# Optimization experiments

Hardware: AMD Instinct MI355X
Metric: run time of the kernel (lower is better)

Reference implementation:

```python
import jax, jax.numpy as jnp
import numpy as np

NUM_LAYER = 3
LEAKY = 0.8
RES = 0.8  # residual scale in convolution


def spmm(row, col, val, x, n):
    # sparse (n x n) COO @ dense (n x d)
    return jax.ops.segment_sum(val[:, None] * x[col], row, num_segments=n)


def convolution(emb, row, col, val):
    n = emb.shape[0]
    all_e = emb
    acc = emb  # layer-0 term
    for _ in range(NUM_LAYER):
        all_e = spmm(row, col, val, all_e, n) + RES * all_e
        acc = acc + all_e
    return acc / (NUM_LAYER + 1)


def setup_inputs() -> dict:
    key = jax.random.key(0)
    ks = jax.random.split(key, 32)
    B, NU, NQ, NC, DE, DF = 16384, 50000, 20000, 512, 64, 128
    EU, EQ, EK = 1600000, 640000, 16384
    inp = {}
    inp['user_id'] = jax.random.randint(ks[0], (B,), 0, NU)
    inp['question_id'] = jax.random.randint(ks[1], (B,), 0, NQ)
    inp['q_table'] = (jax.random.uniform(ks[2], (NQ, NC)) < 0.05).astype(jnp.float32)
    inp['u_row'] = jax.random.randint(ks[3], (EU,), 0, NU)
    inp['u_col'] = jax.random.randint(ks[4], (EU,), 0, NU)
    inp['u_val'] = jax.random.uniform(ks[5], (EU,)) / 32.0
    inp['e_row'] = jax.random.randint(ks[6], (EQ,), 0, NQ)
    inp['e_col'] = jax.random.randint(ks[7], (EQ,), 0, NQ)
    inp['e_val'] = jax.random.uniform(ks[8], (EQ,)) / 32.0
    inp['k_row'] = jax.random.randint(ks[9], (EK,), 0, NC)
    inp['k_col'] = jax.random.randint(ks[10], (EK,), 0, NC)
    inp['k_val'] = jax.random.uniform(ks[11], (EK,)) / 32.0
    inp['student_emb'] = jax.random.normal(ks[12], (NU, DE)) * 0.1
    inp['exercise_emb'] = jax.random.normal(ks[13], (NQ, DE)) * 0.1
    inp['knowledge_emb'] = jax.random.normal(ks[14], (NC, DE)) * 0.1
    inp['W_s'] = jax.random.normal(ks[15], (DE, DF)) * 0.1
    inp['b_s'] = jnp.zeros((DF,))
    inp['W_e'] = jax.random.normal(ks[16], (DE, DF)) * 0.1
    inp['b_e'] = jnp.zeros((DF,))
    inp['W_k'] = jax.random.normal(ks[17], (DE, DF)) * 0.1
    inp['b_k'] = jnp.zeros((DF,))
    inp['W_d'] = jax.random.normal(ks[18], (DE, 1)) * 0.1
    inp['b_d'] = jnp.zeros((1,))
    inp['M1_w'] = jax.random.normal(ks[19], (NC, 512)) * 0.05
    inp['M1_b'] = jnp.zeros((512,))
    inp['M2_w'] = jax.random.normal(ks[20], (512, 256)) * 0.05
    inp['M2_b'] = jnp.zeros((256,))
    inp['M3_w'] = jax.random.normal(ks[21], (256, 128)) * 0.05
    inp['M3_b'] = jnp.zeros((128,))
    inp['M4_w'] = jax.random.normal(ks[22], (128, 1)) * 0.05
    inp['M4_b'] = jnp.zeros((1,))
    return inp


def reference(user_id, question_id, q_table,
              u_row, u_col, u_val, e_row, e_col, e_val, k_row, k_col, k_val,
              student_emb, exercise_emb, knowledge_emb,
              W_s, b_s, W_e, b_e, W_k, b_k, W_d, b_d,
              M1_w, M1_b, M2_w, M2_b, M3_w, M3_b, M4_w, M4_b):
    cs = convolution(student_emb, u_row, u_col, u_val)    # [NU, DE]
    ce = convolution(exercise_emb, e_row, e_col, e_val)   # [NQ, DE]
    ck = convolution(knowledge_emb, k_row, k_col, k_val)  # [NC, DE]
    bs = cs[user_id]        # [B, DE]
    be = ce[question_id]    # [B, DE]
    sf = jax.nn.leaky_relu(bs @ W_s + b_s, LEAKY)   # [B, DF]
    ef = jax.nn.leaky_relu(be @ W_e + b_e, LEAKY)   # [B, DF]
    kf = jax.nn.leaky_relu(ck @ W_k + b_k, LEAKY)   # [NC, DF]
    disc = jax.nn.sigmoid(be @ W_d + b_d)           # [B, 1]
    state = disc * ((sf - ef) @ kf.T) * q_table[question_id]  # [B, NC]
    h = jnp.tanh(state @ M1_w + M1_b)
    h = jnp.tanh(h @ M2_w + M2_b)
    h = jnp.tanh(h @ M3_w + M3_b)
    return jax.nn.sigmoid(h @ M4_w + M4_b).reshape(-1)  # [B]
```

## Files before the change

kernel.cpp:

```cpp
#include <hip/hip_runtime.h>
#include <hip/hip_bf16.h>
#include <math.h>

#define RESF 0.8f
#define LEAKYF 0.8f
#define BWSH 6
#define BWID 64
#define BSTRIDE 2432

typedef __attribute__((ext_vector_type(8))) short bs8;
typedef __attribute__((ext_vector_type(4))) float f32x4;

__device__ __forceinline__ void gload16(const void* g, void* l) {
  __builtin_amdgcn_global_load_lds((const __attribute__((address_space(1))) void*)g,
                                   (__attribute__((address_space(3))) void*)l, 16, 0, 0);
}

__device__ __forceinline__ float tanh_fast(float x) {
  float t = __expf(2.f * x);
  return 1.f - 2.f * __builtin_amdgcn_rcpf(1.f + t);
}
__device__ __forceinline__ float sigmoid_fast(float x) {
  return __builtin_amdgcn_rcpf(1.f + __expf(-x));
}
__device__ __forceinline__ float bf2f(ushort u) {
  return __uint_as_float((unsigned)u << 16);
}
__device__ __forceinline__ ushort f2bf(float a) {
  __hip_bfloat16 h = __float2bfloat16(a);
  return *(ushort*)&h;
}

__device__ __forceinline__ int edge_row(int e, const int* __restrict__ rU, const int* __restrict__ rE,
                                        const int* __restrict__ rK, int EU, int EQ, int NU, int NQ) {
  if (e < EU) return rU[e];
  if ((e -= EU) < EQ) return NU + rE[e];
  e -= EQ;
  return NU + NQ + rK[e];
}

__device__ __forceinline__ void edge_full(int e,
    const int* __restrict__ rU, const int* __restrict__ cU, const float* __restrict__ vU,
    const int* __restrict__ rE, const int* __restrict__ cE, const float* __restrict__ vE,
    const int* __restrict__ rK, const int* __restrict__ cK, const float* __restrict__ vK,
    int EU, int EQ, int NU, int NQ, int& grow, int& gcol, float& val) {
  if (e < EU) { grow = rU[e]; gcol = cU[e]; val = vU[e]; return; }
  if ((e -= EU) < EQ) { grow = NU + rE[e]; gcol = NU + cE[e]; val = vE[e]; return; }
  e -= EQ;
  grow = NU + NQ + rK[e]; gcol = NU + NQ + cK[e]; val = vK[e];
}

__global__ __launch_bounds__(256) void k_setup(int* __restrict__ gcur, int* __restrict__ flags,
                                               int* __restrict__ nneed, int nbuck, int N_tot) {
  int i = blockIdx.x * 256 + threadIdx.x;
  if (i < nbuck) gcur[i] = i * BSTRIDE;
  if (i < N_tot) flags[i] = 0;
  if (i == 0) nneed[0] = 0;
}

__global__ __launch_bounds__(1024) void k_bin(
    const int* __restrict__ rU, const int* __restrict__ cU, const float* __restrict__ vU,
    const int* __restrict__ rE, const int* __restrict__ cE, const float* __restrict__ vE,
    const int* __restrict__ rK, const int* __restrict__ cK, const float* __restrict__ vK,
    int* __restrict__ gcur, int2* __restrict__ tmp,
    int EU, int EQ, int EK, int NU, int NQ, int nbuck, int chunk) {
  extern __shared__ int l[];
  int* lh = l;
  int* lbase = l + nbuck;
  int t = threadIdx.x;
  for (int i = t; i < nbuck; i += 1024) lh[i] = 0;
  __syncthreads();
  int E = EU + EQ + EK;
  int lo = blockIdx.x * chunk;
  int hi = lo + chunk < E ? lo + chunk : E;
  for (int e = lo + t; e < hi; e += 1024) {
    int grow = edge_row(e, rU, rE, rK, EU, EQ, NU, NQ);
    atomicAdd(&lh[grow >> BWSH], 1);
  }
  __syncthreads();
  for (int i = t; i < nbuck; i += 1024) {
    int c = lh[i];
    if (c) lbase[i] = atomicAdd(&gcur[i], c);
    lh[i] = 0;
  }
  __syncthreads();
  for (int e = lo + t; e < hi; e += 1024) {
    int grow, gcol;
    float val;
    edge_full(e, rU, cU, vU, rE, cE, vE, rK, cK, vK, EU, EQ, NU, NQ, grow, gcol, val);
    int b = grow >> BWSH;
    int r = atomicAdd(&lh[b], 1);
    int2 pk;
    pk.x = ((grow & (BWID - 1)) << 26) | gcol;
    pk.y = __float_as_int(val);
    tmp[lbase[b] + r] = pk;
  }
}

__global__ __launch_bounds__(1024) void k_scan2(const int* __restrict__ gcur, int* __restrict__ boff, int n) {
  __shared__ int s[16];
  int tid = threadIdx.x;
  int lane = tid & 63, wid = tid >> 6;
  int carry = 0;
  for (int base = 0; base < n; base += 1024) {
    int i = base + tid;
    int x = (i < n) ? (gcur[i] - i * BSTRIDE) : 0;
    int v = x;
#pragma unroll
    for (int d = 1; d < 64; d <<= 1) {
      int t = __shfl_up(v, d);
      if (lane >= d) v += t;
    }
    if (lane == 63) s[wid] = v;
    __syncthreads();
    if (tid < 16) {
      int w = s[tid];
#pragma unroll
      for (int d = 1; d < 16; d <<= 1) {
        int t = __shfl_up(w, d);
        if (tid >= d) w += t;
      }
      s[tid] = w;
    }
    __syncthreads();
    int wofs = (wid > 0) ? s[wid - 1] : 0;
    int total = s[15];
    if (i < n) boff[i] = carry + wofs + v - x;
    carry += total;
    __syncthreads();
  }
  if (tid == 0) boff[n] = carry;
}

__global__ __launch_bounds__(256) void k_sort(const int2* __restrict__ tmp, int2* __restrict__ sorted,
                                              const int* __restrict__ gcur, const int* __restrict__ boff,
                                              int* __restrict__ roff, int N_tot, int E_tot) {
  __shared__ int cnt[BWID];
  __shared__ int cur[BWID];
  int b = blockIdx.x, t = threadIdx.x;
  int beg = b * BSTRIDE, end = gcur[b];
  int dst = boff[b];
  if (t < BWID) cnt[t] = 0;
  __syncthreads();
  for (int e = beg + t; e < end; e += 256)
    atomicAdd(&cnt[((unsigned)tmp[e].x) >> 26], 1);
  __syncthreads();
  if (t < BWID) {
    int x = cnt[t];
    int v = x;
#pragma unroll
    for (int d = 1; d < 64; d <<= 1) {
      int y = __shfl_up(v, d);
      if (t >= d) v += y;
    }
    cur[t] = v - x;
    int r = (b << BWSH) + t;
    if (r < N_tot) roff[r] = dst + v - x;
  }
  __syncthreads();
  for (int e = beg + t; e < end; e += 256) {
    int2 pe = tmp[e];
    int rl = ((unsigned)pe.x) >> 26;
    int rank = atomicAdd(&cur[rl], 1);
    sorted[dst + rank] = pe;
  }
  if (b == 0 && t == 0) roff[N_tot] = E_tot;
}

__global__ __launch_bounds__(256) void k_flag(const int* __restrict__ user_id,
                                              const int* __restrict__ question_id,
                                              int* __restrict__ flags, int B, int NU) {
  int i = blockIdx.x * 256 + threadIdx.x;
  if (i < B) {
    flags[user_id[i]] = 1;
    flags[NU + question_id[i]] = 1;
  }
}

__global__ __launch_bounds__(256) void k_compact(const int* __restrict__ flags, int* __restrict__ list,
                                                 int* __restrict__ nneed, int N_tot, int NUQ) {
  int i = blockIdx.x * 256 + threadIdx.x;
  if (i >= N_tot) return;
  if (flags[i] || i >= NUQ) {
    int p = atomicAdd(nneed, 1);
    list[p] = i;
  }
}

__global__ __launch_bounds__(256) void k_init3(ushort* __restrict__ lay0,
                                               const float* __restrict__ embU,
                                               const float* __restrict__ embE,
                                               const float* __restrict__ embK,
                                               int n4U, int n4E, int n4K) {
  int n4 = n4U + n4E + n4K;
  int stride = gridDim.x * 256;
  ushort4* c4 = (ushort4*)lay0;
  for (int i = blockIdx.x * 256 + threadIdx.x; i < n4; i += stride) {
    const float4* src;
    int j = i;
    if (j < n4U) src = (const float4*)embU;
    else if ((j -= n4U) < n4E) src = (const float4*)embE;
    else { j -= n4E; src = (const float4*)embK; }
    float4 v = src[j];
    ushort4 u;
    u.x = f2bf(v.x); u.y = f2bf(v.y); u.z = f2bf(v.z); u.w = f2bf(v.w);
    c4[i] = u;
  }
}

__device__ __forceinline__ void spmm_core(const ushort* __restrict__ curb,
                                          const int2* __restrict__ edges,
                                          int beg, int end, int li, int eh,
                                          float& a0, float& a1, float& a2, float& a3) {
  int lane = (eh << 4) | li;
  for (int base = beg; base < end; base += 64) {
    int rem = end - base;
    int m = rem < 64 ? rem : 64;
    int c = 0, vi = 0;
    if (lane < m) {
      int2 pe = edges[base + lane];
      c = pe.x & 0x3FFFFFF;
      vi = pe.y;
    }
    for (int j = 0; j * 4 < m; j += 4) {
      int s0 = (j + 0) * 4 + eh, s1 = (j + 1) * 4 + eh;
      int s2 = (j + 2) * 4 + eh, s3 = (j + 3) * 4 + eh;
      int cc0 = __shfl(c, s0), cc1 = __shfl(c, s1), cc2 = __shfl(c, s2), cc3 = __shfl(c, s3);
      float vf0 = __int_as_float(__shfl(vi, s0));
      float vf1 = __int_as_float(__shfl(vi, s1));
      float vf2 = __int_as_float(__shfl(vi, s2));
      float vf3 = __int_as_float(__shfl(vi, s3));
      uint2 x0 = *(const uint2*)&curb[(size_t)cc0 * 64 + 4 * li];
      uint2 x1 = *(const uint2*)&curb[(size_t)cc1 * 64 + 4 * li];
      uint2 x2 = *(const uint2*)&curb[(size_t)cc2 * 64 + 4 * li];
      uint2 x3 = *(const uint2*)&curb[(size_t)cc3 * 64 + 4 * li];
      a0 = fmaf(vf0, __uint_as_float(x0.x << 16), a0);
      a1 = fmaf(vf0, __uint_as_float(x0.x & 0xffff0000u), a1);
      a2 = fmaf(vf0, __uint_as_float(x0.y << 16), a2);
      a3 = fmaf(vf0, __uint_as_float(x0.y & 0xffff0000u), a3);
      a0 = fmaf(vf1, __uint_as_float(x1.x << 16), a0);
      a1 = fmaf(vf1, __uint_as_float(x1.x & 0xffff0000u), a1);
      a2 = fmaf(vf1, __uint_as_float(x1.y << 16), a2);
      a3 = fmaf(vf1, __uint_as_float(x1.y & 0xffff0000u), a3);
      a0 = fmaf(vf2, __uint_as_float(x2.x << 16), a0);
      a1 = fmaf(vf2, __uint_as_float(x2.x & 0xffff0000u), a1);
      a2 = fmaf(vf2, __uint_as_float(x2.y << 16), a2);
      a3 = fmaf(vf2, __uint_as_float(x2.y & 0xffff0000u), a3);
      a0 = fmaf(vf3, __uint_as_float(x3.x << 16), a0);
      a1 = fmaf(vf3, __uint_as_float(x3.x & 0xffff0000u), a1);
      a2 = fmaf(vf3, __uint_as_float(x3.y << 16), a2);
      a3 = fmaf(vf3, __uint_as_float(x3.y & 0xffff0000u), a3);
    }
  }
  a0 += __shfl_xor(a0, 16); a0 += __shfl_xor(a0, 32);
  a1 += __shfl_xor(a1, 16); a1 += __shfl_xor(a1, 32);
  a2 += __shfl_xor(a2, 16); a2 += __shfl_xor(a2, 32);
  a3 += __shfl_xor(a3, 16); a3 += __shfl_xor(a3, 32);
}

__global__ __launch_bounds__(256) void k_spmm2(const ushort* __restrict__ curb,
                                               ushort* __restrict__ nxtb,
                                               const int* __restrict__ off,
                                               const int2* __restrict__ edges, int n) {
  int r = blockIdx.x * 4 + (threadIdx.x >> 6);
  if (r >= n) return;
  int lane = threadIdx.x & 63;
  int li = lane & 15, eh = lane >> 4;
  int beg = off[r], end = off[r + 1];
  float a0 = 0.f, a1 = 0.f, a2 = 0.f, a3 = 0.f;
  spmm_core(curb, edges, beg, end, li, eh, a0, a1, a2, a3);
  if (eh == 0) {
    size_t gi = (size_t)r * 64 + 4 * li;
    uint2 cv = *(const uint2*)&curb[gi];
    a0 = fmaf(RESF, __uint_as_float(cv.x << 16), a0);
    a1 = fmaf(RESF, __uint_as_float(cv.x & 0xffff0000u), a1);
    a2 = fmaf(RESF, __uint_as_float(cv.y << 16), a2);
    a3 = fmaf(RESF, __uint_as_float(cv.y & 0xffff0000u), a3);
    uint2 o;
    o.x = ((unsigned)f2bf(a1) << 16) | f2bf(a0);
    o.y = ((unsigned)f2bf(a3) << 16) | f2bf(a2);
    *(uint2*)&nxtb[gi] = o;
  }
}

__global__ __launch_bounds__(256) void k_spmm3(const ushort* __restrict__ curb,
                                               const ushort* __restrict__ lay1,
                                               const float* __restrict__ embU,
                                               const float* __restrict__ embE,
                                               const float* __restrict__ embK,
                                               float* __restrict__ acc,
                                               const int* __restrict__ off,
                                               const int2* __restrict__ edges,
                                               const int* __restrict__ list,
                                               const int* __restrict__ nneed,
                                               int NU, int NQ) {
  int idx = blockIdx.x * 4 + (threadIdx.x >> 6);
  if (idx >= *nneed) return;
  int r = list[idx];
  int lane = threadIdx.x & 63;
  int li = lane & 15, eh = lane >> 4;
  int beg = off[r], end = off[r + 1];
  float a0 = 0.f, a1 = 0.f, a2 = 0.f, a3 = 0.f;
  spmm_core(curb, edges, beg, end, li, eh, a0, a1, a2, a3);
  if (eh == 0) {
    size_t gi = (size_t)r * 64 + 4 * li;
    const float* ep;
    if (r < NU) ep = embU + gi;
    else if (r < NU + NQ) ep = embE + (gi - (size_t)NU * 64);
    else ep = embK + (gi - (size_t)(NU + NQ) * 64);
    float4 e = *(const float4*)ep;
    uint2 l1 = *(const uint2*)&lay1[gi];
    uint2 c2 = *(const uint2*)&curb[gi];
    float c20 = __uint_as_float(c2.x << 16);
    float c21 = __uint_as_float(c2.x & 0xffff0000u);
    float c22 = __uint_as_float(c2.y << 16);
    float c23 = __uint_as_float(c2.y & 0xffff0000u);
    float4 o;
    o.x = e.x + __uint_as_float(l1.x << 16) + c20 + fmaf(RESF, c20, a0);
    o.y = e.y + __uint_as_float(l1.x & 0xffff0000u) + c21 + fmaf(RESF, c21, a1);
    o.z = e.z + __uint_as_float(l1.y << 16) + c22 + fmaf(RESF, c22, a2);
    o.w = e.w + __uint_as_float(l1.y & 0xffff0000u) + c23 + fmaf(RESF, c23, a3);
    *(float4*)&acc[gi] = o;
  }
}

__global__ __launch_bounds__(256) void k_prep(const float* __restrict__ acc_k,
                                              const float* __restrict__ W_k, const float* __restrict__ b_k,
                                              __hip_bfloat16* __restrict__ kfb,
                                              const float* __restrict__ M1_w, __hip_bfloat16* __restrict__ W1t,
                                              const float* __restrict__ M2_w, __hip_bfloat16* __restrict__ W2t,
                                              const float* __restrict__ M3_w, __hip_bfloat16* __restrict__ W3t) {
  int idx = blockIdx.x * 256 + threadIdx.x;
  if (idx < 65536) {
    int d = idx & 127, c = idx >> 7;
    float a = b_k[d];
#pragma unroll 8
    for (int k = 0; k < 64; ++k) a += 0.25f * acc_k[c * 64 + k] * W_k[k * 128 + d];
    float v = a > 0.f ? a : LEAKYF * a;
    kfb[c * 128 + d] = __float2bfloat16(v);
    return;
  }
  int j = idx - 65536;
  if (j < 262144) {
    int n = j >> 9, k = j & 511;
    W1t[n * 512 + k] = __float2bfloat16(M1_w[k * 512 + n]);
    return;
  }
  j -= 262144;
  if (j < 131072) {
    int n = j >> 9, k = j & 511;
    W2t[n * 512 + k] = __float2bfloat16(M2_w[k * 256 + n]);
    return;
  }
  j -= 131072;
  if (j < 32768) {
    int n = j >> 8, k = j & 255;
    W3t[n * 256 + k] = __float2bfloat16(M3_w[k * 128 + n]);
  }
}

__global__ __launch_bounds__(256) void k_diff(
    const int* __restrict__ user_id, const int* __restrict__ question_id,
    const float* __restrict__ acc_u, const float* __restrict__ acc_e,
    const float* __restrict__ W_s, const float* __restrict__ b_s,
    const float* __restrict__ W_e, const float* __restrict__ b_e,
    const float* __restrict__ W_d, const float* __restrict__ b_d,
    __hip_bfloat16* __restrict__ diff, float* __restrict__ disc, int B) {
  __shared__ float bs_l[16 * 64];
  __shared__ float be_l[16 * 64];
  int t = threadIdx.x;
  int row0 = blockIdx.x * 16;
  for (int i = t; i < 16 * 64; i += 256) {
    int r = i >> 6, d = i & 63;
    int gb = row0 + r;
    bs_l[i] = 0.25f * acc_u[(size_t)user_id[gb] * 64 + d];
    be_l[i] = 0.25f * acc_e[(size_t)question_id[gb] * 64 + d];
  }
  __syncthreads();

  int j = t & 127, half = t >> 7;
  float as[8], ae[8];
#pragma unroll
  for (int rr = 0; rr < 8; ++rr) { as[rr] = b_s[j]; ae[rr] = b_e[j]; }
#pragma unroll 4
  for (int k = 0; k < 64; ++k) {
    float ws = W_s[k * 128 + j];
    float we = W_e[k * 128 + j];
#pragma unroll
    for (int rr = 0; rr < 8; ++rr) {
      as[rr] = fmaf(bs_l[(half * 8 + rr) * 64 + k], ws, as[rr]);
      ae[rr] = fmaf(be_l[(half * 8 + rr) * 64 + k], we, ae[rr]);
    }
  }
#pragma unroll
  for (int rr = 0; rr < 8; ++rr) {
    float sfv = as[rr] > 0.f ? as[rr] : LEAKYF * as[rr];
    float efv = ae[rr] > 0.f ? ae[rr] : LEAKYF * ae[rr];
    diff[(size_t)(row0 + half * 8 + rr) * 128 + j] = __float2bfloat16(sfv - efv);
  }
  if (t < 16) {
    float a = b_d[0];
#pragma unroll 8
    for (int k = 0; k < 64; ++k) a = fmaf(be_l[t * 64 + k], W_d[k], a);
    disc[row0 + t] = sigmoid_fast(a);
  }
}

template <int K, int MODE>
__global__ __launch_bounds__(256) void k_gemm(
    const __hip_bfloat16* __restrict__ A, const __hip_bfloat16* __restrict__ Bw,
    __hip_bfloat16* __restrict__ C, int N,
    const float* __restrict__ bias,
    const float* __restrict__ disc, const int* __restrict__ qid,
    const float* __restrict__ q_table) {
  __shared__ __align__(16) short lA[128 * 32];
  __shared__ __align__(16) short lB[128 * 32];
  __shared__ float s_disc[128];
  __shared__ int s_qid[128];
  __shared__ float s_bias[128];

  int t = threadIdx.x;
  int lane = t & 63;
  int w = t >> 6;
  int wr = (w >> 1) * 64, wc = (w & 1) * 64;
  int bm0 = blockIdx.y * 128, bn0 = blockIdx.x * 128;

  if (MODE == 0) {
    if (t < 128) {
      s_disc[t] = disc[bm0 + t];
      s_qid[t] = qid[bm0 + t];
    }
  } else {
    if (t < 128) s_bias[t] = bias[bn0 + t];
  }

  int off0 = t, off1 = 256 + t;
  int rA0 = off0 >> 2, gq0 = (off0 & 3) ^ ((rA0 >> 1) & 3);
  int rA1 = off1 >> 2, gq1 = (off1 & 3) ^ ((rA1 >> 1) & 3);

  const __hip_bfloat16* Ab = A + (size_t)bm0 * K;
  const __hip_bfloat16* Bb = Bw + (size_t)bn0 * K;

  f32x4 acc[4][4] = {};
  int q = lane >> 4, fr = lane & 15;

  for (int k0 = 0; k0 < K; k0 += 32) {
    __syncthreads();
    gload16(Ab + (size_t)rA0 * K + k0 + gq0 * 8, lA + (size_t)off0 * 8);
    gload16(Ab + (size_t)rA1 * K + k0 + gq1 * 8, lA + (size_t)off1 * 8);
    gload16(Bb + (size_t)rA0 * K + k0 + gq0 * 8, lB + (size_t)off0 * 8);
    gload16(Bb + (size_t)rA1 * K + k0 + gq1 * 8, lB + (size_t)off1 * 8);
    __syncthreads();

    bs8 af[4], bf[4];
#pragma unroll
    for (int mi = 0; mi < 4; ++mi) {
      int row = wr + mi * 16 + fr;
      int a16 = row * 4 + (q ^ ((row >> 1) & 3));
      af[mi] = *(const bs8*)&lA[a16 * 8];
    }
#pragma unroll
    for (int ni = 0; ni < 4; ++ni) {
      int col = wc + ni * 16 + fr;
      int b16 = col * 4 + (q ^ ((col >> 1) & 3));
      bf[ni] = *(const bs8*)&lB[b16 * 8];
    }
#pragma unroll
    for (int mi = 0; mi < 4; ++mi)
#pragma unroll
      for (int ni = 0; ni < 4; ++ni)
        acc[mi][ni] = __builtin_amdgcn_mfma_f32_16x16x32_bf16(af[mi], bf[ni], acc[mi][ni], 0, 0, 0);
  }

#pragma unroll
  for (int mi = 0; mi < 4; ++mi) {
    int lr0 = wr + mi * 16 + q * 4;
#pragma unroll
    for (int j = 0; j < 4; ++j) {
      int lr = lr0 + j;
      size_t gr = bm0 + lr;
      float dsc = 0.f;
      size_t qrow = 0;
      if (MODE == 0) {
        dsc = s_disc[lr];
        qrow = (size_t)s_qid[lr] * 512;
      }
#pragma unroll
      for (int ni = 0; ni < 4; ++ni) {
        int lc = wc + ni * 16 + fr;
        int gc = bn0 + lc;
        float v = acc[mi][ni][j];
        if (MODE == 0) {
          v = dsc * v * q_table[qrow + gc];
        } else {
          v = tanh_fast(v + s_bias[lc]);
        }
        C[gr * N + gc] = __float2bfloat16(v);
      }
    }
  }
}

__global__ __launch_bounds__(256) void k_out(const __hip_bfloat16* __restrict__ h3,
                                             const float* __restrict__ M4_w, const float* __restrict__ M4_b,
                                             float* __restrict__ out, int B) {
  __shared__ float sM4[128];
  int t = threadIdx.x;
  if (t < 128) sM4[t] = M4_w[t];
  __syncthreads();
  int w = t >> 6, l = t & 63;
  int row = blockIdx.x * 16 + w * 4 + (l >> 4);
  int k0 = (l & 15) * 8;
  const ushort* hp = (const ushort*)(h3 + (size_t)row * 128 + k0);
  float p = 0.f;
#pragma unroll
  for (int i = 0; i < 8; ++i) {
    float x = __uint_as_float((unsigned)hp[i] << 16);
    p = fmaf(x, sM4[k0 + i], p);
  }
#pragma unroll
  for (int off = 8; off; off >>= 1) p += __shfl_xor(p, off, 16);
  if ((l & 15) == 0 && row < B) out[row] = sigmoid_fast(p + M4_b[0]);
}

static inline int iminh(int a, int b) { return a < b ? a : b; }
static inline size_t rnd4(size_t x) { return (x + 3) & ~(size_t)3; }

extern "C" void kernel_launch(void* const* d_in, const int* in_sizes, int n_in,
                              void* d_out, int out_size, void* d_ws, size_t ws_size,
                              hipStream_t stream) {
  const int* user_id = (const int*)d_in[0];
  const int* question_id = (const int*)d_in[1];
  const float* q_table = (const float*)d_in[2];
  const int* u_row = (const int*)d_in[3];
  const int* u_col = (const int*)d_in[4];
  const float* u_val = (const float*)d_in[5];
  const int* e_row = (const int*)d_in[6];
  const int* e_col = (const int*)d_in[7];
  const float* e_val = (const float*)d_in[8];
  const int* k_row = (const int*)d_in[9];
  const int* k_col = (const int*)d_in[10];
  const float* k_val = (const float*)d_in[11];
  const float* student_emb = (const float*)d_in[12];
  const float* exercise_emb = (const float*)d_in[13];
  const float* knowledge_emb = (const float*)d_in[14];
  const float* W_s = (const float*)d_in[15];
  const float* b_s = (const float*)d_in[16];
  const float* W_e = (const float*)d_in[17];
  const float* b_e = (const float*)d_in[18];
  const float* W_k = (const float*)d_in[19];
  const float* b_k = (const float*)d_in[20];
  const float* W_d = (const float*)d_in[21];
  const float* b_d = (const float*)d_in[22];
  const float* M1_w = (const float*)d_in[23];
  const float* M1_b = (const float*)d_in[24];
  const float* M2_w = (const float*)d_in[25];
  const float* M2_b = (const float*)d_in[26];
  const float* M3_w = (const float*)d_in[27];
  const float* M3_b = (const float*)d_in[28];
  const float* M4_w = (const float*)d_in[29];
  const float* M4_b = (const float*)d_in[30];

  int B = in_sizes[0];
  int NU = in_sizes[12] / 64;
  int NQ = in_sizes[13] / 64;
  int NC = in_sizes[14] / 64;
  int EU = in_sizes[3];
  int EQ = in_sizes[6];
  int EK = in_sizes[9];
  int N_tot = NU + NQ + NC;
  int E_tot = EU + EQ + EK;
  int nbuck = (N_tot + BWID - 1) >> BWSH;

  float* w = (float*)d_ws;
  float* acc = w; w += rnd4((size_t)N_tot * 64);
  __hip_bfloat16* kfb = (__hip_bfloat16*)w; w += rnd4(512 * 128 / 2);
  float* U = w;

  float* acc_u = acc;
  float* acc_e = acc + (size_t)NU * 64;
  float* acc_k = acc + (size_t)(NU + NQ) * 64;

  float* cw = U;
  ushort* lay0 = (ushort*)cw; cw += rnd4((size_t)N_tot * 32);
  ushort* lay1 = (ushort*)cw; cw += rnd4((size_t)N_tot * 32);
  int2* sorted = (int2*)cw;   cw += rnd4((size_t)E_tot * 2);
  int* gcur = (int*)cw;  cw += rnd4(nbuck);
  int* boff = (int*)cw;  cw += rnd4(nbuck + 1);
  int* roff = (int*)cw;  cw += rnd4(N_tot + 1);
  int* flags = (int*)cw; cw += rnd4(N_tot);
  int* list = (int*)cw;  cw += rnd4(N_tot);
  int* nneed = (int*)cw; cw += rnd4(4);
  float* alias0 = cw;
  int2* tmp = (int2*)alias0;
  ushort* lay2 = (ushort*)alias0;
  {
    size_t tmp_f = rnd4((size_t)nbuck * BSTRIDE * 2);
    size_t lay_f = rnd4((size_t)N_tot * 32);
    cw += (tmp_f > lay_f ? tmp_f : lay_f);
  }

  float* mw = U;
  __hip_bfloat16* W1t = (__hip_bfloat16*)mw; mw += rnd4(512 * 512 / 2);
  __hip_bfloat16* W2t = (__hip_bfloat16*)mw; mw += rnd4(256 * 512 / 2);
  __hip_bfloat16* W3t = (__hip_bfloat16*)mw; mw += rnd4(128 * 256 / 2);
  __hip_bfloat16* diff = (__hip_bfloat16*)mw; mw += rnd4((size_t)B * 128 / 2);
  float* disc = mw; mw += rnd4(B);
  __hip_bfloat16* state = (__hip_bfloat16*)mw; mw += rnd4((size_t)B * 512 / 2);
  __hip_bfloat16* h1 = (__hip_bfloat16*)mw;    mw += rnd4((size_t)B * 512 / 2);
  __hip_bfloat16* h2 = state;
  __hip_bfloat16* h3 = diff;

  {
    int gs = 256;
    int chunk = (E_tot + gs - 1) / gs;
    k_setup<<<(N_tot + 255) / 256, 256, 0, stream>>>(gcur, flags, nneed, nbuck, N_tot);
    k_bin<<<gs, 1024, nbuck * 8, stream>>>(u_row, u_col, u_val, e_row, e_col, e_val,
                                           k_row, k_col, k_val, gcur, tmp,
                                           EU, EQ, EK, NU, NQ, nbuck, chunk);
    k_scan2<<<1, 1024, 0, stream>>>(gcur, boff, nbuck);
    k_sort<<<nbuck, 256, 0, stream>>>(tmp, sorted, gcur, boff, roff, N_tot, E_tot);
  }

  k_flag<<<(B + 255) / 256, 256, 0, stream>>>(user_id, question_id, flags, B, NU);
  k_compact<<<(N_tot + 255) / 256, 256, 0, stream>>>(flags, list, nneed, N_tot, NU + NQ);

  {
    int n4 = N_tot * 16;
    int gs = iminh((n4 + 255) / 256, 2048);
    k_init3<<<gs, 256, 0, stream>>>(lay0, student_emb, exercise_emb, knowledge_emb,
                                    NU * 16, NQ * 16, NC * 16);
    k_spmm2<<<(N_tot + 3) / 4, 256, 0, stream>>>(lay0, lay1, roff, sorted, N_tot);
    k_spmm2<<<(N_tot + 3) / 4, 256, 0, stream>>>(lay1, lay2, roff, sorted, N_tot);
    int maxneed = iminh(2 * B + NC, N_tot);
    k_spmm3<<<(maxneed + 3) / 4, 256, 0, stream>>>(lay2, lay1, student_emb, exercise_emb,
                                                   knowledge_emb, acc, roff, sorted,
                                                   list, nneed, NU, NQ);
  }

  k_prep<<<(65536 + 262144 + 131072 + 32768) / 256, 256, 0, stream>>>(
      acc_k, W_k, b_k, kfb, M1_w, W1t, M2_w, W2t, M3_w, W3t);

  k_diff<<<B / 16, 256, 0, stream>>>(user_id, question_id, acc_u, acc_e,
                                     W_s, b_s, W_e, b_e, W_d, b_d, diff, disc, B);

  k_gemm<128, 0><<<dim3(512 / 128, B / 128), 256, 0, stream>>>(
      diff, kfb, state, 512, nullptr, disc, question_id, q_table);
  k_gemm<512, 1><<<dim3(512 / 128, B / 128), 256, 0, stream>>>(
      state, W1t, h1, 512, M1_b, nullptr, nullptr, nullptr);
  k_gemm<512, 1><<<dim3(256 / 128, B / 128), 256, 0, stream>>>(
      h1, W2t, h2, 256, M2_b, nullptr, nullptr, nullptr);
  k_gemm<256, 1><<<dim3(128 / 128, B / 128), 256, 0, stream>>>(
      h2, W3t, h3, 128, M3_b, nullptr, nullptr, nullptr);

  k_out<<<B / 16, 256, 0, stream>>>(h3, M4_w, M4_b, (float*)d_out, B);
}
```

Measured before the change: 245.0 us.

## Stage binned edges in LDS and scatter bucket-contiguous to global memory

The binning kernel now reads each edge once into registers, counts per-bucket in LDS, does a block-wide prefix scan, and places the packed edges in LDS sorted by bucket before writing them out in bucket-contiguous runs. Before, it read the row arrays twice and wrote each edge to a random global position. Chunks are fixed at 5120 edges, which gives many more blocks. The goal is to cut the duplicate reads and make the global writes coalesced. In exchange it uses more LDS per block and adds a scan whose cost grows with the bucket count.

```diff
diff --git a/kernel.cpp b/kernel.cpp
--- a/kernel.cpp
+++ b/kernel.cpp
@@ -7,6 +7,8 @@
 #define BWSH 6
 #define BWID 64
 #define BSTRIDE 2432
+#define BINCH 5120
+#define BINR 5
 
 typedef __attribute__((ext_vector_type(8))) short bs8;
 typedef __attribute__((ext_vector_type(4))) float f32x4;
@@ -29,14 +31,6 @@
 __device__ __forceinline__ ushort f2bf(float a) {
   __hip_bfloat16 h = __float2bfloat16(a);
   return *(ushort*)&h;
-}
-
-__device__ __forceinline__ int edge_row(int e, const int* __restrict__ rU, const int* __restrict__ rE,
-                                        const int* __restrict__ rK, int EU, int EQ, int NU, int NQ) {
-  if (e < EU) return rU[e];
-  if ((e -= EU) < EQ) return NU + rE[e];
-  e -= EQ;
-  return NU + NQ + rK[e];
 }
 
 __device__ __forceinline__ void edge_full(int e,
@@ -63,37 +57,89 @@
     const int* __restrict__ rE, const int* __restrict__ cE, const float* __restrict__ vE,
     const int* __restrict__ rK, const int* __restrict__ cK, const float* __restrict__ vK,
     int* __restrict__ gcur, int2* __restrict__ tmp,
-    int EU, int EQ, int EK, int NU, int NQ, int nbuck, int chunk) {
+    int EU, int EQ, int EK, int NU, int NQ, int nbuck) {
   extern __shared__ int l[];
-  int* lh = l;
-  int* lbase = l + nbuck;
+  int metaN = (2 * nbuck + 3) & ~3;
+  int* cnt = l;
+  int* dstb = l + nbuck;
+  int2* spk = (int2*)(l + metaN);
+  ushort* sbk = (ushort*)(spk + BINCH);
+  __shared__ int wsum[16];
+
   int t = threadIdx.x;
-  for (int i = t; i < nbuck; i += 1024) lh[i] = 0;
+  int lane = t & 63, wid = t >> 6;
+  for (int i = t; i < nbuck; i += 1024) cnt[i] = 0;
   __syncthreads();
+
   int E = EU + EQ + EK;
-  int lo = blockIdx.x * chunk;
-  int hi = lo + chunk < E ? lo + chunk : E;
-  for (int e = lo + t; e < hi; e += 1024) {
-    int grow = edge_row(e, rU, rE, rK, EU, EQ, NU, NQ);
-    atomicAdd(&lh[grow >> BWSH], 1);
+  int lo = blockIdx.x * BINCH;
+  int hi = lo + BINCH < E ? lo + BINCH : E;
+  int m = hi - lo;
+
+  int2 pk[BINR];
+  int bk[BINR];
+#pragma unroll
+  for (int k = 0; k < BINR; ++k) {
+    int e = lo + t + k * 1024;
+    bk[k] = -1;
+    if (e < hi) {
+      int grow, gcol;
+      float val;
+      edge_full(e, rU, cU, vU, rE, cE, vE, rK, cK, vK, EU, EQ, NU, NQ, grow, gcol, val);
+      pk[k].x = ((grow & (BWID - 1)) << 26) | gcol;
+      pk[k].y = __float_as_int(val);
+      int b = grow >> BWSH;
+      bk[k] = b;
+      atomicAdd(&cnt[b], 1);
+    }
   }
   __syncthreads();
-  for (int i = t; i < nbuck; i += 1024) {
-    int c = lh[i];
-    if (c) lbase[i] = atomicAdd(&gcur[i], c);
-    lh[i] = 0;
+
+  int carry = 0;
+  for (int base = 0; base < nbuck; base += 1024) {
+    int i = base + t;
+    int x = (i < nbuck) ? cnt[i] : 0;
+    int v = x;
+#pragma unroll
+    for (int d = 1; d < 64; d <<= 1) {
+      int y = __shfl_up(v, d);
+      if (lane >= d) v += y;
+    }
+    if (lane == 63) wsum[wid] = v;
+    __syncthreads();
+    if (t < 16) {
+      int w = wsum[t];
+#pragma unroll
+      for (int d = 1; d < 16; d <<= 1) {
+        int y = __shfl_up(w, d);
+        if (t >= d) w += y;
+      }
+      wsum[t] = w;
+    }
+    __syncthreads();
+    int excl = carry + ((wid > 0) ? wsum[wid - 1] : 0) + v - x;
+    if (i < nbuck) {
+      int gb = x ? atomicAdd(&gcur[i], x) : 0;
+      dstb[i] = gb - excl;
+      cnt[i] = excl;
+    }
+    carry += wsum[15];
+    __syncthreads();
+  }
+
+#pragma unroll
+  for (int k = 0; k < BINR; ++k) {
+    if (bk[k] >= 0) {
+      int p = atomicAdd(&cnt[bk[k]], 1);
+      spk[p] = pk[k];
+      sbk[p] = (ushort)bk[k];
+    }
   }
   __syncthreads();
-  for (int e = lo + t; e < hi; e += 1024) {
-    int grow, gcol;
-    float val;
-    edge_full(e, rU, cU, vU, rE, cE, vE, rK, cK, vK, EU, EQ, NU, NQ, grow, gcol, val);
-    int b = grow >> BWSH;
-    int r = atomicAdd(&lh[b], 1);
-    int2 pk;
-    pk.x = ((grow & (BWID - 1)) << 26) | gcol;
-    pk.y = __float_as_int(val);
-    tmp[lbase[b] + r] = pk;
+
+  for (int i = t; i < m; i += 1024) {
+    int b = sbk[i];
+    tmp[dstb[b] + i] = spk[i];
   }
 }
 
@@ -612,12 +658,13 @@
   __hip_bfloat16* h3 = diff;
 
   {
-    int gs = 256;
-    int chunk = (E_tot + gs - 1) / gs;
+    int gsb = (E_tot + BINCH - 1) / BINCH;
+    int metaN = (2 * nbuck + 3) & ~3;
+    size_t ldsb = (size_t)metaN * 4 + (size_t)BINCH * 8 + (size_t)BINCH * 2;
     k_setup<<<(N_tot + 255) / 256, 256, 0, stream>>>(gcur, flags, nneed, nbuck, N_tot);
-    k_bin<<<gs, 1024, nbuck * 8, stream>>>(u_row, u_col, u_val, e_row, e_col, e_val,
-                                           k_row, k_col, k_val, gcur, tmp,
-                                           EU, EQ, EK, NU, NQ, nbuck, chunk);
+    k_bin<<<gsb, 1024, ldsb, stream>>>(u_row, u_col, u_val, e_row, e_col, e_val,
+                                       k_row, k_col, k_val, gcur, tmp,
+                                       EU, EQ, EK, NU, NQ, nbuck);
     k_scan2<<<1, 1024, 0, stream>>>(gcur, boff, nbuck);
     k_sort<<<nbuck, 256, 0, stream>>>(tmp, sorted, gcur, boff, roff, N_tot, E_tot);
   }
```

Result: faster. 237.7 us (-3.0%).
